# Performance work log

Hardware: AMD Instinct MI355X
Metric: run time of the kernel (lower is better)

## Reference

```python
import jax, jax.numpy as jnp
import numpy as np

B, N, DIM = 4, 2048, 1024
H, DH = 16, 64
INNER = H * DH  # 1024
SCALE = DH ** -0.5


def setup_inputs() -> dict:
    key = jax.random.key(0)
    ks = jax.random.split(key, 6)
    s = 0.02
    return {
        "x": jax.random.normal(ks[0], (B, N, DIM), dtype=jnp.float32),
        "Wq": jax.random.normal(ks[1], (DIM, INNER), dtype=jnp.float32) * s,
        "Wk": jax.random.normal(ks[2], (DIM, INNER), dtype=jnp.float32) * s,
        "Wv": jax.random.normal(ks[3], (DIM, INNER), dtype=jnp.float32) * s,
        "Wo": jax.random.normal(ks[4], (INNER, DIM), dtype=jnp.float32) * s,
        "bo": jax.random.normal(ks[5], (DIM,), dtype=jnp.float32) * s,
    }


def reference(x, Wq, Wk, Wv, Wo, bo):
    # q/k/v projections: [B,N,INNER] -> [B,H,N,DH]
    def split_heads(t):
        return t.reshape(B, N, H, DH).transpose(0, 2, 1, 3)

    q = split_heads(x @ Wq)
    k = split_heads(x @ Wk)
    v = split_heads(x @ Wv)

    # scores [B,H,N,N], scaled dot product, softmax over keys (last dim)
    dots = jnp.einsum('bhid,bhjd->bhij', q, k) * SCALE
    attn = jax.nn.softmax(dots, axis=-1)

    out = jnp.einsum('bhij,bhjd->bhid', attn, v)
    out = out.transpose(0, 2, 1, 3).reshape(B, N, INNER)
    return out @ Wo + bo
```

## Files before the change

### kernel.cpp

```cpp
#include <hip/hip_runtime.h>

#define B_SZ   4
#define N_SEQ  2048
#define DIM    1024
#define H_N    16
#define DH     64
#define INNER  1024
#define M_TOK  8192
#define QSCALE 0.1803368801111244f

typedef __attribute__((ext_vector_type(8))) short bf16x8;
typedef __attribute__((ext_vector_type(4))) float f32x4;

__device__ __forceinline__ unsigned short f2b(float f) {
  union { float f; unsigned u; } v; v.f = f;
  unsigned r = v.u + 0x7fffu + ((v.u >> 16) & 1u);
  return (unsigned short)(r >> 16);
}

__device__ __forceinline__ void gl_lds16(const unsigned short* g, unsigned short* l) {
  __builtin_amdgcn_global_load_lds((const __attribute__((address_space(1))) void*)g,
                                   (__attribute__((address_space(3))) void*)l, 16, 0, 0);
}

__global__ __launch_bounds__(256) void cast_x(const float* __restrict__ x,
                                              unsigned short* __restrict__ xb) {
  int i = (blockIdx.x * 256 + threadIdx.x) * 4;
  float4 v = *(const float4*)(x + i);
  ushort4 o;
  o.x = f2b(v.x); o.y = f2b(v.y); o.z = f2b(v.z); o.w = f2b(v.w);
  *(ushort4*)(xb + i) = o;
}

__global__ __launch_bounds__(256) void trans_w(const float* __restrict__ Wq,
    const float* __restrict__ Wk, const float* __restrict__ Wv,
    const float* __restrict__ Wo, unsigned short* __restrict__ WT) {
  const int z = blockIdx.z;
  const float* W = (z == 0) ? Wq : (z == 1) ? Wk : (z == 2) ? Wv : Wo;
  unsigned short* T = WT + (size_t)z * DIM * INNER;
  __shared__ float tile[64][65];
  const int n0 = blockIdx.x * 64, k0 = blockIdx.y * 64;
  const int tid = threadIdx.x;
#pragma unroll
  for (int it = 0; it < 16; it++) {
    int lin = it * 256 + tid;
    int r = lin >> 6, c = lin & 63;
    tile[r][c] = W[(size_t)(k0 + r) * 1024 + n0 + c];
  }
  __syncthreads();
#pragma unroll
  for (int it = 0; it < 16; it++) {
    int lin = it * 256 + tid;
    int r = lin >> 6, c = lin & 63;
    T[(size_t)(n0 + r) * 1024 + k0 + c] = f2b(tile[c][r]);
  }
}

__global__ __launch_bounds__(256) void qkv_gemm(const unsigned short* __restrict__ xb,
    const unsigned short* __restrict__ WT, unsigned short* __restrict__ QKV) {
  __shared__ __align__(16) unsigned short As[2 * 128 * 32];
  __shared__ __align__(16) unsigned short Bs[2 * 128 * 32];
  const int tid = threadIdx.x;
  const int lane = tid & 63, wv = tid >> 6;
  const int quad = lane >> 4, l16 = lane & 15;
  const int wm = wv >> 1, wn = wv & 1;
  const int m0 = blockIdx.x * 128, n0 = blockIdx.y * 128;
  const unsigned short* Ag = xb + (size_t)m0 * DIM;
  const unsigned short* Bg = WT + (size_t)blockIdx.z * DIM * INNER + (size_t)n0 * DIM;
  unsigned short* Out = QKV + (size_t)blockIdx.z * M_TOK * INNER;

  f32x4 zero = {0.f, 0.f, 0.f, 0.f};
  f32x4 acc[4][4];
#pragma unroll
  for (int i = 0; i < 4; i++)
#pragma unroll
    for (int j = 0; j < 4; j++) acc[i][j] = zero;

  const int lr = lane >> 2, lc = (lane & 3) * 8;
  const int c0 = wv * 2, c1 = wv * 2 + 1;

  for (int k0 = 0; k0 < DIM; k0 += 64) {
    __syncthreads();
#pragma unroll
    for (int h = 0; h < 2; h++) {
      gl_lds16(&Ag[(size_t)(c0 * 16 + lr) * DIM + k0 + h * 32 + lc], &As[h * 4096 + c0 * 512]);
      gl_lds16(&Ag[(size_t)(c1 * 16 + lr) * DIM + k0 + h * 32 + lc], &As[h * 4096 + c1 * 512]);
      gl_lds16(&Bg[(size_t)(c0 * 16 + lr) * DIM + k0 + h * 32 + lc], &Bs[h * 4096 + c0 * 512]);
      gl_lds16(&Bg[(size_t)(c1 * 16 + lr) * DIM + k0 + h * 32 + lc], &Bs[h * 4096 + c1 * 512]);
    }
    __syncthreads();
#pragma unroll
    for (int h = 0; h < 2; h++) {
      bf16x8 af[4], bfr[4];
#pragma unroll
      for (int i = 0; i < 4; i++)
        af[i] = *(const bf16x8*)&As[h * 4096 + (wm * 64 + i * 16 + l16) * 32 + quad * 8];
#pragma unroll
      for (int j = 0; j < 4; j++)
        bfr[j] = *(const bf16x8*)&Bs[h * 4096 + (wn * 64 + j * 16 + l16) * 32 + quad * 8];
#pragma unroll
      for (int i = 0; i < 4; i++)
#pragma unroll
        for (int j = 0; j < 4; j++)
          acc[i][j] = __builtin_amdgcn_mfma_f32_16x16x32_bf16(af[i], bfr[j], acc[i][j], 0, 0, 0);
    }
  }
  if (blockIdx.z != 2) {
    const float cs = (blockIdx.z == 0) ? QSCALE : 1.0f;
#pragma unroll
    for (int i = 0; i < 4; i++) {
#pragma unroll
      for (int j = 0; j < 4; j++) {
        int n = n0 + wn * 64 + j * 16 + l16;
#pragma unroll
        for (int r = 0; r < 4; r++) {
          int m = m0 + wm * 64 + i * 16 + quad * 4 + r;
          Out[(size_t)m * INNER + n] = f2b(acc[i][j][r] * cs);
        }
      }
    }
  } else {
#pragma unroll
    for (int i = 0; i < 4; i++) {
#pragma unroll
      for (int j = 0; j < 4; j++) {
        int n = n0 + wn * 64 + j * 16 + l16;
        int h = n >> 6, dh = n & 63;
        int mbase = m0 + wm * 64 + i * 16 + quad * 4;
        int b = mbase >> 11, nq = mbase & 2047;
        unsigned lo = (unsigned)f2b(acc[i][j][0]) | ((unsigned)f2b(acc[i][j][1]) << 16);
        unsigned hi = (unsigned)f2b(acc[i][j][2]) | ((unsigned)f2b(acc[i][j][3]) << 16);
        uint2 pw; pw.x = lo; pw.y = hi;
        *(uint2*)&Out[((size_t)(b * H_N + h) * DH + dh) * N_SEQ + nq] = pw;
      }
    }
  }
}

#define KT 64
#define LSTR 72

__global__ __launch_bounds__(256, 4) void attn(const unsigned short* __restrict__ Q,
    const unsigned short* __restrict__ K, const unsigned short* __restrict__ VT,
    unsigned short* __restrict__ O) {
  __shared__ __align__(16) unsigned short Ks[KT * LSTR];
  __shared__ __align__(16) unsigned short VTs[DH * LSTR];
  __shared__ __align__(16) unsigned short Ps[128 * LSTR];
  const int tid = threadIdx.x;
  const int lane = tid & 63, w = tid >> 6;
  const int quad = lane >> 4, l16 = lane & 15;
  const int qh = w & 1, kh = w >> 1;
  const int bh = blockIdx.y;
  const int b = bh >> 4, h = bh & 15;
  const int q0 = blockIdx.x * 128;
  const unsigned short* Qp = Q + ((size_t)b * N_SEQ) * INNER + h * DH;
  const unsigned short* Kp = K + ((size_t)b * N_SEQ) * INNER + h * DH;
  const unsigned short* VTp = VT + (size_t)bh * DH * N_SEQ;

  bf16x8 aq[4][2];
#pragma unroll
  for (int qi = 0; qi < 4; qi++) {
    const unsigned short* qr = Qp + (size_t)(q0 + qh * 64 + qi * 16 + l16) * INNER;
    aq[qi][0] = *(const bf16x8*)&qr[quad * 8];
    aq[qi][1] = *(const bf16x8*)&qr[32 + quad * 8];
  }

  bf16x8 vone;
#pragma unroll
  for (int j = 0; j < 8; j++) vone[j] = (short)0x3F80;

  f32x4 zero = {0.f, 0.f, 0.f, 0.f};
  f32x4 oacc[2][4];
  f32x4 lacc[2];
#pragma unroll
  for (int mi = 0; mi < 2; mi++) {
    lacc[mi] = zero;
#pragma unroll
    for (int t = 0; t < 4; t++) oacc[mi][t] = zero;
  }

  const int srow = tid >> 3, scol = (tid & 7) * 8;

  for (int k0 = 0; k0 < N_SEQ; k0 += KT) {
    __syncthreads();
#pragma unroll
    for (int p = 0; p < 2; p++)
      *(uint4*)&Ks[(p * 32 + srow) * LSTR + scol] =
          *(const uint4*)&Kp[(size_t)(k0 + p * 32 + srow) * INNER + scol];
#pragma unroll
    for (int p = 0; p < 2; p++)
      *(uint4*)&VTs[(p * 32 + srow) * LSTR + scol] =
          *(const uint4*)&VTp[(size_t)(p * 32 + srow) * N_SEQ + k0 + scol];
    __syncthreads();

    f32x4 s[2][4];
#pragma unroll
    for (int t = 0; t < 2; t++)
#pragma unroll
      for (int qi = 0; qi < 4; qi++) s[t][qi] = zero;
#pragma unroll
    for (int kk = 0; kk < 2; kk++) {
#pragma unroll
      for (int t = 0; t < 2; t++) {
        bf16x8 ka = *(const bf16x8*)&Ks[(kh * 32 + t * 16 + l16) * LSTR + kk * 32 + quad * 8];
#pragma unroll
        for (int qi = 0; qi < 4; qi++)
          s[t][qi] = __builtin_amdgcn_mfma_f32_16x16x32_bf16(ka, aq[qi][kk], s[t][qi], 0, 0, 0);
      }
    }

#pragma unroll
    for (int t = 0; t < 2; t++) {
#pragma unroll
      for (int qi = 0; qi < 4; qi++) {
#pragma unroll
        for (int r = 0; r < 4; r++)
          s[t][qi][r] = __builtin_amdgcn_exp2f(s[t][qi][r]);
        unsigned lo = (__float_as_uint(s[t][qi][0]) >> 16) |
                      (__float_as_uint(s[t][qi][1]) & 0xffff0000u);
        unsigned hi = (__float_as_uint(s[t][qi][2]) >> 16) |
                      (__float_as_uint(s[t][qi][3]) & 0xffff0000u);
        uint2 pw; pw.x = lo; pw.y = hi;
        *(uint2*)&Ps[(qh * 64 + qi * 16 + l16) * LSTR + kh * 32 + t * 16 + quad * 4] = pw;
      }
    }
    __syncthreads();

#pragma unroll
    for (int kk2 = 0; kk2 < 2; kk2++) {
      bf16x8 pf0 = *(const bf16x8*)&Ps[(w * 32 + l16) * LSTR + kk2 * 32 + quad * 8];
      bf16x8 pf1 = *(const bf16x8*)&Ps[(w * 32 + 16 + l16) * LSTR + kk2 * 32 + quad * 8];
      lacc[0] = __builtin_amdgcn_mfma_f32_16x16x32_bf16(pf0, vone, lacc[0], 0, 0, 0);
      lacc[1] = __builtin_amdgcn_mfma_f32_16x16x32_bf16(pf1, vone, lacc[1], 0, 0, 0);
#pragma unroll
      for (int t2 = 0; t2 < 4; t2++) {
        bf16x8 vf = *(const bf16x8*)&VTs[(t2 * 16 + l16) * LSTR + kk2 * 32 + quad * 8];
        oacc[0][t2] = __builtin_amdgcn_mfma_f32_16x16x32_bf16(pf0, vf, oacc[0][t2], 0, 0, 0);
        oacc[1][t2] = __builtin_amdgcn_mfma_f32_16x16x32_bf16(pf1, vf, oacc[1][t2], 0, 0, 0);
      }
    }
  }

#pragma unroll
  for (int mi = 0; mi < 2; mi++) {
#pragma unroll
    for (int r = 0; r < 4; r++) {
      float rl = __builtin_amdgcn_rcpf(lacc[mi][r]);
      int qrow = q0 + w * 32 + mi * 16 + quad * 4 + r;
#pragma unroll
      for (int t2 = 0; t2 < 4; t2++) {
        int col = h * DH + t2 * 16 + l16;
        O[((size_t)b * N_SEQ + qrow) * INNER + col] = f2b(oacc[mi][t2][r] * rl);
      }
    }
  }
}

__global__ __launch_bounds__(256) void out_gemm(const unsigned short* __restrict__ Ob,
    const unsigned short* __restrict__ WoT, const float* __restrict__ bo,
    float* __restrict__ out) {
  __shared__ __align__(16) unsigned short As[2 * 128 * 32];
  __shared__ __align__(16) unsigned short Bs[2 * 64 * 32];
  const int tid = threadIdx.x;
  const int lane = tid & 63, wv = tid >> 6;
  const int quad = lane >> 4, l16 = lane & 15;
  const int wm = wv >> 1, wn = wv & 1;
  const int m0 = blockIdx.x * 128, n0 = blockIdx.y * 64;
  const unsigned short* Ag = Ob + (size_t)m0 * INNER;
  const unsigned short* Bg = WoT + (size_t)n0 * INNER;

  f32x4 zero = {0.f, 0.f, 0.f, 0.f};
  f32x4 acc[4][2];
#pragma unroll
  for (int i = 0; i < 4; i++)
#pragma unroll
    for (int j = 0; j < 2; j++) acc[i][j] = zero;

  const int lr = lane >> 2, lc = (lane & 3) * 8;
  const int c0 = wv * 2, c1 = wv * 2 + 1;
  const int cb = wv;

  for (int k0 = 0; k0 < INNER; k0 += 64) {
    __syncthreads();
#pragma unroll
    for (int h = 0; h < 2; h++) {
      gl_lds16(&Ag[(size_t)(c0 * 16 + lr) * INNER + k0 + h * 32 + lc], &As[h * 4096 + c0 * 512]);
      gl_lds16(&Ag[(size_t)(c1 * 16 + lr) * INNER + k0 + h * 32 + lc], &As[h * 4096 + c1 * 512]);
      gl_lds16(&Bg[(size_t)(cb * 16 + lr) * INNER + k0 + h * 32 + lc], &Bs[h * 2048 + cb * 512]);
    }
    __syncthreads();
#pragma unroll
    for (int h = 0; h < 2; h++) {
      bf16x8 af[4], bfr[2];
#pragma unroll
      for (int i = 0; i < 4; i++)
        af[i] = *(const bf16x8*)&As[h * 4096 + (wm * 64 + i * 16 + l16) * 32 + quad * 8];
#pragma unroll
      for (int j = 0; j < 2; j++)
        bfr[j] = *(const bf16x8*)&Bs[h * 2048 + (wn * 32 + j * 16 + l16) * 32 + quad * 8];
#pragma unroll
      for (int i = 0; i < 4; i++)
#pragma unroll
        for (int j = 0; j < 2; j++)
          acc[i][j] = __builtin_amdgcn_mfma_f32_16x16x32_bf16(af[i], bfr[j], acc[i][j], 0, 0, 0);
    }
  }
#pragma unroll
  for (int i = 0; i < 4; i++) {
#pragma unroll
    for (int j = 0; j < 2; j++) {
      int n = n0 + wn * 32 + j * 16 + l16;
      float bias = bo[n];
#pragma unroll
      for (int r = 0; r < 4; r++) {
        int m = m0 + wm * 64 + i * 16 + quad * 4 + r;
        out[(size_t)m * DIM + n] = acc[i][j][r] + bias;
      }
    }
  }
}

extern "C" void kernel_launch(void* const* d_in, const int* in_sizes, int n_in,
                              void* d_out, int out_size, void* d_ws, size_t ws_size,
                              hipStream_t stream) {
  const float* x  = (const float*)d_in[0];
  const float* Wq = (const float*)d_in[1];
  const float* Wk = (const float*)d_in[2];
  const float* Wv = (const float*)d_in[3];
  const float* Wo = (const float*)d_in[4];
  const float* bo = (const float*)d_in[5];

  char* ws = (char*)d_ws;
  unsigned short* xb   = (unsigned short*)ws;
  unsigned short* WT   = (unsigned short*)(ws + (size_t)16777216);
  unsigned short* QKV  = (unsigned short*)(ws + (size_t)25165824);
  unsigned short* Obuf = (unsigned short*)(ws + (size_t)75497472);

  cast_x<<<dim3(8192), 256, 0, stream>>>(x, xb);
  trans_w<<<dim3(16, 16, 4), 256, 0, stream>>>(Wq, Wk, Wv, Wo, WT);
  qkv_gemm<<<dim3(64, 8, 3), 256, 0, stream>>>(xb, WT, QKV);
  attn<<<dim3(16, 64), 256, 0, stream>>>(QKV,
                                         QKV + (size_t)M_TOK * INNER,
                                         QKV + (size_t)2 * M_TOK * INNER,
                                         Obuf);
  out_gemm<<<dim3(64, 16), 256, 0, stream>>>(Obuf, WT + (size_t)3 * DIM * INNER, bo,
                                             (float*)d_out);
}
```

Measured before the change: 283.2 us.

## Keep P in registers via permlane swaps and double-buffer K/V tiles

The attention kernel no longer writes the exponentiated score tile to shared memory. Each wave now computes scores for its own 32 query rows against all keys, packs them with v_cvt_pk_bf16_f32, and uses permlane32/16 swaps to rearrange the MFMA output layout into A-operand layout for the PV product. This removes the Ps LDS buffer and one barrier per tile. K/V tiles are double-buffered in LDS with register prefetch of the next tile, leaving a single barrier per iteration. In exchange, each wave now reads all K rows from LDS, and the conversion switches from truncation to round-to-nearest.

```diff
diff --git a/kernel.cpp b/kernel.cpp
--- a/kernel.cpp
+++ b/kernel.cpp
@@ -16,6 +16,12 @@
   union { float f; unsigned u; } v; v.f = f;
   unsigned r = v.u + 0x7fffu + ((v.u >> 16) & 1u);
   return (unsigned short)(r >> 16);
+}
+
+__device__ __forceinline__ unsigned cvtpk_bf16(float a, float b) {
+  unsigned r;
+  asm("v_cvt_pk_bf16_f32 %0, %1, %2" : "=v"(r) : "v"(a), "v"(b));
+  return r;
 }
 
 __device__ __forceinline__ void gl_lds16(const unsigned short* g, unsigned short* l) {
@@ -143,13 +149,11 @@
 __global__ __launch_bounds__(256, 4) void attn(const unsigned short* __restrict__ Q,
     const unsigned short* __restrict__ K, const unsigned short* __restrict__ VT,
     unsigned short* __restrict__ O) {
-  __shared__ __align__(16) unsigned short Ks[KT * LSTR];
-  __shared__ __align__(16) unsigned short VTs[DH * LSTR];
-  __shared__ __align__(16) unsigned short Ps[128 * LSTR];
+  __shared__ __align__(16) unsigned short Ks[2][KT * LSTR];
+  __shared__ __align__(16) unsigned short VTs[2][DH * LSTR];
   const int tid = threadIdx.x;
   const int lane = tid & 63, w = tid >> 6;
   const int quad = lane >> 4, l16 = lane & 15;
-  const int qh = w & 1, kh = w >> 1;
   const int bh = blockIdx.y;
   const int b = bh >> 4, h = bh & 15;
   const int q0 = blockIdx.x * 128;
@@ -157,10 +161,10 @@
   const unsigned short* Kp = K + ((size_t)b * N_SEQ) * INNER + h * DH;
   const unsigned short* VTp = VT + (size_t)bh * DH * N_SEQ;
 
-  bf16x8 aq[4][2];
-#pragma unroll
-  for (int qi = 0; qi < 4; qi++) {
-    const unsigned short* qr = Qp + (size_t)(q0 + qh * 64 + qi * 16 + l16) * INNER;
+  bf16x8 aq[2][2];
+#pragma unroll
+  for (int qi = 0; qi < 2; qi++) {
+    const unsigned short* qr = Qp + (size_t)(q0 + w * 32 + qi * 16 + l16) * INNER;
     aq[qi][0] = *(const bf16x8*)&qr[quad * 8];
     aq[qi][1] = *(const bf16x8*)&qr[32 + quad * 8];
   }
@@ -173,84 +177,101 @@
   f32x4 oacc[2][4];
   f32x4 lacc[2];
 #pragma unroll
-  for (int mi = 0; mi < 2; mi++) {
-    lacc[mi] = zero;
-#pragma unroll
-    for (int t = 0; t < 4; t++) oacc[mi][t] = zero;
+  for (int qi = 0; qi < 2; qi++) {
+    lacc[qi] = zero;
+#pragma unroll
+    for (int t = 0; t < 4; t++) oacc[qi][t] = zero;
   }
 
   const int srow = tid >> 3, scol = (tid & 7) * 8;
 
-  for (int k0 = 0; k0 < N_SEQ; k0 += KT) {
-    __syncthreads();
-#pragma unroll
-    for (int p = 0; p < 2; p++)
-      *(uint4*)&Ks[(p * 32 + srow) * LSTR + scol] =
-          *(const uint4*)&Kp[(size_t)(k0 + p * 32 + srow) * INNER + scol];
-#pragma unroll
-    for (int p = 0; p < 2; p++)
-      *(uint4*)&VTs[(p * 32 + srow) * LSTR + scol] =
-          *(const uint4*)&VTp[(size_t)(p * 32 + srow) * N_SEQ + k0 + scol];
-    __syncthreads();
-
-    f32x4 s[2][4];
-#pragma unroll
-    for (int t = 0; t < 2; t++)
-#pragma unroll
-      for (int qi = 0; qi < 4; qi++) s[t][qi] = zero;
-#pragma unroll
-    for (int kk = 0; kk < 2; kk++) {
-#pragma unroll
-      for (int t = 0; t < 2; t++) {
-        bf16x8 ka = *(const bf16x8*)&Ks[(kh * 32 + t * 16 + l16) * LSTR + kk * 32 + quad * 8];
-#pragma unroll
-        for (int qi = 0; qi < 4; qi++)
-          s[t][qi] = __builtin_amdgcn_mfma_f32_16x16x32_bf16(ka, aq[qi][kk], s[t][qi], 0, 0, 0);
-      }
-    }
-
-#pragma unroll
-    for (int t = 0; t < 2; t++) {
-#pragma unroll
-      for (int qi = 0; qi < 4; qi++) {
-#pragma unroll
-        for (int r = 0; r < 4; r++)
-          s[t][qi][r] = __builtin_amdgcn_exp2f(s[t][qi][r]);
-        unsigned lo = (__float_as_uint(s[t][qi][0]) >> 16) |
-                      (__float_as_uint(s[t][qi][1]) & 0xffff0000u);
-        unsigned hi = (__float_as_uint(s[t][qi][2]) >> 16) |
-                      (__float_as_uint(s[t][qi][3]) & 0xffff0000u);
-        uint2 pw; pw.x = lo; pw.y = hi;
-        *(uint2*)&Ps[(qh * 64 + qi * 16 + l16) * LSTR + kh * 32 + t * 16 + quad * 4] = pw;
-      }
-    }
-    __syncthreads();
-
-#pragma unroll
-    for (int kk2 = 0; kk2 < 2; kk2++) {
-      bf16x8 pf0 = *(const bf16x8*)&Ps[(w * 32 + l16) * LSTR + kk2 * 32 + quad * 8];
-      bf16x8 pf1 = *(const bf16x8*)&Ps[(w * 32 + 16 + l16) * LSTR + kk2 * 32 + quad * 8];
-      lacc[0] = __builtin_amdgcn_mfma_f32_16x16x32_bf16(pf0, vone, lacc[0], 0, 0, 0);
-      lacc[1] = __builtin_amdgcn_mfma_f32_16x16x32_bf16(pf1, vone, lacc[1], 0, 0, 0);
+  uint4 kreg[2], vreg[2];
+#pragma unroll
+  for (int p = 0; p < 2; p++) {
+    kreg[p] = *(const uint4*)&Kp[(size_t)(p * 32 + srow) * INNER + scol];
+    vreg[p] = *(const uint4*)&VTp[(size_t)(p * 32 + srow) * N_SEQ + scol];
+  }
+
+  const int NT = N_SEQ / KT;
+  for (int it = 0; it < NT; it++) {
+    unsigned short* ks = Ks[it & 1];
+    unsigned short* vs = VTs[it & 1];
+#pragma unroll
+    for (int p = 0; p < 2; p++) {
+      *(uint4*)&ks[(p * 32 + srow) * LSTR + scol] = kreg[p];
+      *(uint4*)&vs[(p * 32 + srow) * LSTR + scol] = vreg[p];
+    }
+    __syncthreads();
+    if (it + 1 < NT) {
+      const int kn = (it + 1) * KT;
+#pragma unroll
+      for (int p = 0; p < 2; p++) {
+        kreg[p] = *(const uint4*)&Kp[(size_t)(kn + p * 32 + srow) * INNER + scol];
+        vreg[p] = *(const uint4*)&VTp[(size_t)(p * 32 + srow) * N_SEQ + kn + scol];
+      }
+    }
+
+#pragma unroll
+    for (int half = 0; half < 2; half++) {
+      f32x4 s[2][2];
+#pragma unroll
+      for (int t = 0; t < 2; t++)
+#pragma unroll
+        for (int qi = 0; qi < 2; qi++) s[t][qi] = zero;
+
+#pragma unroll
+      for (int kk = 0; kk < 2; kk++) {
+#pragma unroll
+        for (int t = 0; t < 2; t++) {
+          bf16x8 ka = *(const bf16x8*)&ks[((half * 2 + t) * 16 + l16) * LSTR + kk * 32 + quad * 8];
+#pragma unroll
+          for (int qi = 0; qi < 2; qi++)
+            s[t][qi] = __builtin_amdgcn_mfma_f32_16x16x32_bf16(ka, aq[qi][kk], s[t][qi], 0, 0, 0);
+        }
+      }
+
+      bf16x8 pa[2];
+#pragma unroll
+      for (int qi = 0; qi < 2; qi++) {
+#pragma unroll
+        for (int t = 0; t < 2; t++)
+#pragma unroll
+          for (int r = 0; r < 4; r++)
+            s[t][qi][r] = __builtin_amdgcn_exp2f(s[t][qi][r]);
+        unsigned lo0 = cvtpk_bf16(s[0][qi][0], s[0][qi][1]);
+        unsigned hi0 = cvtpk_bf16(s[0][qi][2], s[0][qi][3]);
+        unsigned lo1 = cvtpk_bf16(s[1][qi][0], s[1][qi][1]);
+        unsigned hi1 = cvtpk_bf16(s[1][qi][2], s[1][qi][3]);
+        asm("v_permlane32_swap_b32 %0, %1" : "+v"(lo0), "+v"(lo1));
+        asm("v_permlane16_swap_b32 %0, %1" : "+v"(lo0), "+v"(lo1));
+        asm("v_permlane32_swap_b32 %0, %1" : "+v"(hi0), "+v"(hi1));
+        asm("v_permlane16_swap_b32 %0, %1" : "+v"(hi0), "+v"(hi1));
+        union { unsigned u[4]; bf16x8 v; } pk;
+        pk.u[0] = lo0; pk.u[1] = hi0; pk.u[2] = lo1; pk.u[3] = hi1;
+        pa[qi] = pk.v;
+      }
+
+      lacc[0] = __builtin_amdgcn_mfma_f32_16x16x32_bf16(pa[0], vone, lacc[0], 0, 0, 0);
+      lacc[1] = __builtin_amdgcn_mfma_f32_16x16x32_bf16(pa[1], vone, lacc[1], 0, 0, 0);
 #pragma unroll
       for (int t2 = 0; t2 < 4; t2++) {
-        bf16x8 vf = *(const bf16x8*)&VTs[(t2 * 16 + l16) * LSTR + kk2 * 32 + quad * 8];
-        oacc[0][t2] = __builtin_amdgcn_mfma_f32_16x16x32_bf16(pf0, vf, oacc[0][t2], 0, 0, 0);
-        oacc[1][t2] = __builtin_amdgcn_mfma_f32_16x16x32_bf16(pf1, vf, oacc[1][t2], 0, 0, 0);
-      }
-    }
-  }
-
-#pragma unroll
-  for (int mi = 0; mi < 2; mi++) {
+        bf16x8 vf = *(const bf16x8*)&vs[(t2 * 16 + l16) * LSTR + half * 32 + quad * 8];
+        oacc[0][t2] = __builtin_amdgcn_mfma_f32_16x16x32_bf16(pa[0], vf, oacc[0][t2], 0, 0, 0);
+        oacc[1][t2] = __builtin_amdgcn_mfma_f32_16x16x32_bf16(pa[1], vf, oacc[1][t2], 0, 0, 0);
+      }
+    }
+  }
+
+#pragma unroll
+  for (int qi = 0; qi < 2; qi++) {
 #pragma unroll
     for (int r = 0; r < 4; r++) {
-      float rl = __builtin_amdgcn_rcpf(lacc[mi][r]);
-      int qrow = q0 + w * 32 + mi * 16 + quad * 4 + r;
+      float rl = __builtin_amdgcn_rcpf(lacc[qi][r]);
+      int qrow = q0 + w * 32 + qi * 16 + quad * 4 + r;
 #pragma unroll
       for (int t2 = 0; t2 < 4; t2++) {
         int col = h * DH + t2 * 16 + l16;
-        O[((size_t)b * N_SEQ + qrow) * INNER + col] = f2b(oacc[mi][t2][r] * rl);
+        O[((size_t)b * N_SEQ + qrow) * INNER + col] = f2b(oacc[qi][t2][r] * rl);
       }
     }
   }
```

Measured after the change: 345.4 us. 22.0% more time.
